# Kernel tuning notes

Measured on AMD Instinct MI355X. Metric: run time of the kernel, lower is better.

## Reference

```python
import jax, jax.numpy as jnp
import numpy as np

NUM_HEADS = 8


def setup_inputs() -> dict:
    key = jax.random.key(0)
    ks = jax.random.split(key, 14)
    B, S, E = 4, 2048, 512
    D_EMO = 64
    s = 1.0 / np.sqrt(E)
    inp = {
        "query": jax.random.normal(ks[0], (B, S, E), jnp.float32),
        "key": jax.random.normal(ks[1], (B, S, E), jnp.float32),
        "value": jax.random.normal(ks[2], (B, S, E), jnp.float32),
        "emotional_context": jax.random.normal(ks[3], (B, D_EMO), jnp.float32),
        "Wq": jax.random.normal(ks[4], (E, E), jnp.float32) * s,
        "bq": jnp.zeros((E,), jnp.float32),
        "Wk": jax.random.normal(ks[5], (E, E), jnp.float32) * s,
        "bk": jnp.zeros((E,), jnp.float32),
        "Wv": jax.random.normal(ks[6], (E, E), jnp.float32) * s,
        "bv": jnp.zeros((E,), jnp.float32),
        "Wo": jax.random.normal(ks[7], (E, E), jnp.float32) * s,
        "bo": jnp.zeros((E,), jnp.float32),
        "emo_bias": jax.random.normal(ks[8], (NUM_HEADS, 1, 1), jnp.float32),
    }
    return inp


def reference(query, key, value, emotional_context, Wq, bq, Wk, bk, Wv, bv, Wo, bo, emo_bias):
    B, S, E = query.shape
    H = NUM_HEADS
    D = E // H
    scale = 1.0 / np.sqrt(D).astype(np.float32)

    def proj(x, W, b):  # [B,S,E] -> [B,H,S,D]
        return (x @ W.T + b).reshape(B, S, H, D).transpose(0, 2, 1, 3)

    Q = proj(query, Wq, bq)
    K = proj(key, Wk, bk)
    V = proj(value, Wv, bv)

    # [B,H,S,S] score tensor (the memory-bound hot spot)
    scores = jnp.einsum("bhqd,bhkd->bhqk", Q, K) * scale
    scores = scores + emo_bias[None]  # additive per-head emotional bias
    # multiplicative emotional modulation: sigmoid of mean context, per batch
    mod = 0.5 + 0.5 * jax.nn.sigmoid(emotional_context.mean(axis=-1))  # [B]
    scores = scores * mod[:, None, None, None]

    attn = jax.nn.softmax(scores, axis=-1)
    # dropout(0.1) is identity in eval mode
    attended = jnp.einsum("bhqk,bhkd->bhqd", attn, V)
    attended = attended.transpose(0, 2, 1, 3).reshape(B, S, E)
    output = attended @ Wo.T + bo
    return output, attn.mean(axis=1)
```

## Files before the change

### kernel.cpp

```cpp
#include <hip/hip_runtime.h>

#define BATCH 4
#define SEQ   2048
#define EMB   512
#define HEADS 8
#define HD    64

typedef _Float16 half2_t __attribute__((ext_vector_type(2)));
typedef _Float16 half4_t __attribute__((ext_vector_type(4)));
typedef _Float16 half8_t __attribute__((ext_vector_type(8)));
typedef float    f32x4   __attribute__((ext_vector_type(4)));

#if __has_builtin(__builtin_amdgcn_exp2f)
#define EXP2F(x) __builtin_amdgcn_exp2f(x)
#else
#define EXP2F(x) exp2f(x)
#endif
#define LOG2E 1.44269504088896f

#define PKRTZ(a, b) __builtin_bit_cast(half2_t, __builtin_amdgcn_cvt_pkrtz((a), (b)))

__global__ void mod_kernel(const float* __restrict__ emo, float* __restrict__ modv){
    int lane = threadIdx.x;
    for (int b = 0; b < BATCH; ++b){
        float v = emo[b*64 + lane];
        #pragma unroll
        for (int off = 32; off >= 1; off >>= 1) v += __shfl_xor(v, off, 64);
        if (lane == 0){
            float mean = v * (1.0f/64.0f);
            float sig  = 1.0f/(1.0f + __expf(-mean));
            modv[b] = 0.5f + 0.5f*sig;
        }
    }
}

__device__ inline half8_t cvt8pk(float4 v0, float4 v1){
    half2_t p0 = PKRTZ(v0.x, v0.y), p1 = PKRTZ(v0.z, v0.w);
    half2_t p2 = PKRTZ(v1.x, v1.y), p3 = PKRTZ(v1.z, v1.w);
    half4_t a = __builtin_shufflevector(p0, p1, 0, 1, 2, 3);
    half4_t b = __builtin_shufflevector(p2, p3, 0, 1, 2, 3);
    return __builtin_shufflevector(a, b, 0, 1, 2, 3, 4, 5, 6, 7);
}
__device__ inline half8_t cvt8(const float* p){
    return cvt8pk(*(const float4*)p, *(const float4*)(p + 4));
}

__global__ __launch_bounds__(256) void qkv_kernel(
    const float* __restrict__ X0, const float* __restrict__ X1, const float* __restrict__ X2,
    const float* __restrict__ W0, const float* __restrict__ W1, const float* __restrict__ W2,
    const float* __restrict__ b0, const float* __restrict__ b1, const float* __restrict__ b2,
    _Float16* __restrict__ o0, _Float16* __restrict__ o1, _Float16* __restrict__ o2)
{
    const int z = blockIdx.z;
    const float* X    = (z==0) ? X0 : (z==1) ? X1 : X2;
    const float* W    = (z==0) ? W0 : (z==1) ? W1 : W2;
    const float* bias = (z==0) ? b0 : (z==1) ? b1 : b2;
    _Float16*  out    = (z==0) ? o0 : (z==1) ? o1 : o2;

    __shared__ _Float16 lA[128*64];
    __shared__ _Float16 lB[64*64];

    const int tid  = threadIdx.x;
    const int wid  = tid >> 6;
    const int lane = tid & 63;
    const int l16  = lane & 15;
    const int g    = lane >> 4;
    const int l7   = l16 & 7;
    const int mb = blockIdx.x;
    const int nb = blockIdx.y;
    const int wm = (wid >> 1)*64;
    const int wn = (wid & 1)*32;
    const int tR = tid >> 3;
    const int c8 = tid & 7;

    #pragma unroll
    for (int p = 0; p < 4; ++p){
        const int R = p*32 + tR;
        *(half8_t*)(lA + R*64 + ((c8 ^ (R & 7))*8)) = cvt8(X + (size_t)(mb*128 + R)*EMB + c8*8);
    }
    #pragma unroll
    for (int p = 0; p < 2; ++p){
        const int R = p*32 + tR;
        *(half8_t*)(lB + R*64 + ((c8 ^ (R & 7))*8)) = cvt8(W + (size_t)(nb*64 + R)*EMB + c8*8);
    }
    __syncthreads();

    f32x4 acc[4][2] = {};
    for (int ks = 0; ks < 8; ++ks){
        float4 xa0[4], xa1[4], wb0[2], wb1[2];
        if (ks < 7){
            #pragma unroll
            for (int p = 0; p < 4; ++p){
                const float* px = X + (size_t)(mb*128 + p*32 + tR)*EMB + (ks+1)*64 + c8*8;
                xa0[p] = *(const float4*)px;
                xa1[p] = *(const float4*)(px + 4);
            }
            #pragma unroll
            for (int p = 0; p < 2; ++p){
                const float* pw = W + (size_t)(nb*64 + p*32 + tR)*EMB + (ks+1)*64 + c8*8;
                wb0[p] = *(const float4*)pw;
                wb1[p] = *(const float4*)(pw + 4);
            }
        }
        __builtin_amdgcn_s_setprio(1);
        #pragma unroll
        for (int u = 0; u < 2; ++u){
            half8_t af[4], bf[2];
            #pragma unroll
            for (int i = 0; i < 4; ++i){
                const int rA = wm + i*16 + l16;
                af[i] = *(half8_t*)(lA + rA*64 + (((u*4 + g) ^ l7)*8));
            }
            #pragma unroll
            for (int j = 0; j < 2; ++j){
                const int rB = wn + j*16 + l16;
                bf[j] = *(half8_t*)(lB + rB*64 + (((u*4 + g) ^ l7)*8));
            }
            #pragma unroll
            for (int i = 0; i < 4; ++i)
                #pragma unroll
                for (int j = 0; j < 2; ++j)
                    acc[i][j] = __builtin_amdgcn_mfma_f32_16x16x32_f16(af[i], bf[j], acc[i][j], 0, 0, 0);
        }
        __builtin_amdgcn_s_setprio(0);
        __syncthreads();
        if (ks < 7){
            #pragma unroll
            for (int p = 0; p < 4; ++p){
                const int R = p*32 + tR;
                *(half8_t*)(lA + R*64 + ((c8 ^ (R & 7))*8)) = cvt8pk(xa0[p], xa1[p]);
            }
            #pragma unroll
            for (int p = 0; p < 2; ++p){
                const int R = p*32 + tR;
                *(half8_t*)(lB + R*64 + ((c8 ^ (R & 7))*8)) = cvt8pk(wb0[p], wb1[p]);
            }
            __syncthreads();
        }
    }
    #pragma unroll
    for (int j = 0; j < 2; ++j){
        const int nn  = nb*64 + wn + j*16 + l16;
        const float bn = bias[nn];
        const int h = nn >> 6, d = nn & 63;
        #pragma unroll
        for (int i = 0; i < 4; ++i){
            #pragma unroll
            for (int r = 0; r < 4; ++r){
                const int m  = mb*128 + wm + i*16 + 4*g + r;
                const int bb2 = m >> 11, s = m & 2047;
                const int bh  = bb2*8 + h;
                const float v = acc[i][j][r] + bn;
                size_t idx;
                if (z == 2)
                    idx = ((size_t)(bh*128 + (s>>4))*2 + (d>>5))*512
                        + (size_t)((((s>>2)&3)*16 + (d&15))*8 + ((d>>4)&1)*4 + (s&3));
                else
                    idx = ((size_t)(bh*128 + (s>>4))*2 + (d>>5))*512
                        + (size_t)((((d>>3)&3)*16 + (s&15))*8 + (d&7));
                out[idx] = (_Float16)v;
            }
        }
    }
}

__global__ __launch_bounds__(256) void pv_kernel(
    const _Float16* __restrict__ Qf, const _Float16* __restrict__ Kf,
    const _Float16* __restrict__ Vf, const float* __restrict__ emo_bias,
    const float* __restrict__ modv, _Float16* __restrict__ attended,
    float* __restrict__ Ldenom)
{
    __shared__ _Float16 lK[2][4096];
    __shared__ _Float16 lV[2][4096];

    const int tid  = threadIdx.x;
    const int lane = tid & 63;
    const int l16  = lane & 15;
    const int g    = lane >> 4;
    const int n    = blockIdx.x;
    const int work = (n & 7)*128 + (n >> 3);
    const int qt   = work & 31;
    const int bh   = work >> 5;
    const int b    = bh >> 3, h = bh & 7;
    const int q0   = qt*64 + (tid >> 6)*16;

    const float mod = modv[b];
    const float sm2 = 0.125f * mod * LOG2E;
    const float bm2 = emo_bias[h] * mod * LOG2E;

    const size_t fB = (size_t)bh * 128;

    half8_t qf[2];
    #pragma unroll
    for (int c = 0; c < 2; ++c)
        qf[c] = *(const half8_t*)(Qf + ((fB + (q0>>4))*2 + c)*512 + lane*8);

    {
        const _Float16* gk = Kf + fB*1024;
        const _Float16* gv = Vf + fB*1024;
        *(half8_t*)(&lK[0][tid*8])        = *(const half8_t*)(gk + tid*8);
        *(half8_t*)(&lK[0][2048 + tid*8]) = *(const half8_t*)(gk + 2048 + tid*8);
        *(half8_t*)(&lV[0][tid*8])        = *(const half8_t*)(gv + tid*8);
        *(half8_t*)(&lV[0][2048 + tid*8]) = *(const half8_t*)(gv + 2048 + tid*8);
    }
    __syncthreads();

    const half4_t ones4 = {(_Float16)1.0f, (_Float16)1.0f, (_Float16)1.0f, (_Float16)1.0f};
    f32x4 acc[4] = {};
    f32x4 acc5 = {};
    int cur = 0;
    for (int grp = 0; grp < SEQ/64; ++grp){
        half8_t rk0, rk1, rv0, rv1;
        if (grp < SEQ/64 - 1){
            const _Float16* gk = Kf + (fB + (size_t)(grp+1)*4)*1024;
            const _Float16* gv = Vf + (fB + (size_t)(grp+1)*4)*1024;
            rk0 = *(const half8_t*)(gk + tid*8);
            rk1 = *(const half8_t*)(gk + 2048 + tid*8);
            rv0 = *(const half8_t*)(gv + tid*8);
            rv1 = *(const half8_t*)(gv + 2048 + tid*8);
        }
        const _Float16* kb = &lK[cur][0];
        const _Float16* vb = &lV[cur][0];
        f32x4 s[4];
        __builtin_amdgcn_s_setprio(1);
        #pragma unroll
        for (int t = 0; t < 4; ++t){
            half8_t k0 = *(const half8_t*)(kb + (t*2+0)*512 + lane*8);
            half8_t k1 = *(const half8_t*)(kb + (t*2+1)*512 + lane*8);
            f32x4 zz = {};
            zz = __builtin_amdgcn_mfma_f32_16x16x32_f16(k0, qf[0], zz, 0, 0, 0);
            zz = __builtin_amdgcn_mfma_f32_16x16x32_f16(k1, qf[1], zz, 0, 0, 0);
            s[t] = zz;
        }
        __builtin_amdgcn_s_setprio(0);
        half4_t pf[4];
        #pragma unroll
        for (int t = 0; t < 4; ++t){
            float e0 = EXP2F(s[t][0]*sm2 + bm2);
            float e1 = EXP2F(s[t][1]*sm2 + bm2);
            float e2 = EXP2F(s[t][2]*sm2 + bm2);
            float e3 = EXP2F(s[t][3]*sm2 + bm2);
            half2_t plo = PKRTZ(e0, e1), phi = PKRTZ(e2, e3);
            pf[t] = __builtin_shufflevector(plo, phi, 0, 1, 2, 3);
        }
        __builtin_amdgcn_s_setprio(1);
        #pragma unroll
        for (int t = 0; t < 4; ++t){
            half8_t vp0 = *(const half8_t*)(vb + (t*2+0)*512 + lane*8);
            half8_t vp1 = *(const half8_t*)(vb + (t*2+1)*512 + lane*8);
            half4_t v0 = __builtin_shufflevector(vp0, vp0, 0, 1, 2, 3);
            half4_t v1 = __builtin_shufflevector(vp0, vp0, 4, 5, 6, 7);
            half4_t v2 = __builtin_shufflevector(vp1, vp1, 0, 1, 2, 3);
            half4_t v3 = __builtin_shufflevector(vp1, vp1, 4, 5, 6, 7);
            acc5   = __builtin_amdgcn_mfma_f32_16x16x16f16(pf[t], ones4, acc5, 0, 0, 0);
            acc[0] = __builtin_amdgcn_mfma_f32_16x16x16f16(pf[t], v0, acc[0], 0, 0, 0);
            acc[1] = __builtin_amdgcn_mfma_f32_16x16x16f16(pf[t], v1, acc[1], 0, 0, 0);
            acc[2] = __builtin_amdgcn_mfma_f32_16x16x16f16(pf[t], v2, acc[2], 0, 0, 0);
            acc[3] = __builtin_amdgcn_mfma_f32_16x16x16f16(pf[t], v3, acc[3], 0, 0, 0);
        }
        __builtin_amdgcn_s_setprio(0);
        if (grp < SEQ/64 - 1){
            *(half8_t*)(&lK[cur^1][tid*8])        = rk0;
            *(half8_t*)(&lK[cur^1][2048 + tid*8]) = rk1;
            *(half8_t*)(&lV[cur^1][tid*8])        = rv0;
            *(half8_t*)(&lV[cur^1][2048 + tid*8]) = rv1;
        }
        __syncthreads();
        cur ^= 1;
    }

    if (l16 == 0){
        #pragma unroll
        for (int r = 0; r < 4; ++r)
            Ldenom[(size_t)bh*SEQ + q0 + 4*g + r] = acc5[r];
    }
    float invr[4];
    #pragma unroll
    for (int r = 0; r < 4; ++r)
        invr[r] = 1.0f / acc5[r];
    #pragma unroll
    for (int c = 0; c < 4; ++c)
        #pragma unroll
        for (int r = 0; r < 4; ++r)
            attended[(size_t)(b*SEQ + q0 + 4*g + r)*EMB + h*64 + 16*c + l16]
                = (_Float16)(acc[c][r] * invr[r]);
}

__global__ __launch_bounds__(256) void mean_kernel(
    const _Float16* __restrict__ Qf, const _Float16* __restrict__ Kf,
    const float* __restrict__ emo_bias, const float* __restrict__ modv,
    const float* __restrict__ Ldenom, float* __restrict__ mean_out)
{
    const int tid  = threadIdx.x;
    const int w    = tid >> 6;
    const int lane = tid & 63;
    const int l16  = lane & 15;
    const int g    = lane >> 4;
    const int n    = blockIdx.x;
    const int work = (n & 7)*256 + (n >> 3);
    const int b    = work >> 9;
    const int ky   = (work >> 6) & 7;
    const int qt   = work & 63;
    const int q0   = qt * 32;
    const int k0w  = ky*256 + w*64;

    const float mod = modv[b];
    const float sm2 = 0.125f * mod * LOG2E;

    f32x4 msum[2][4] = {};
    for (int hp = 0; hp < HEADS/2; ++hp){
        const int h0 = 2*hp, h1 = 2*hp + 1;
        const size_t lo0 = (size_t)(b*HEADS + h0) * SEQ;
        const size_t lo1 = (size_t)(b*HEADS + h1) * SEQ;
        const size_t f0  = (size_t)(b*HEADS + h0) * 128;
        const size_t f1  = (size_t)(b*HEADS + h1) * 128;
        const float bm20 = emo_bias[h0] * mod * LOG2E;
        const float bm21 = emo_bias[h1] * mod * LOG2E;
        half8_t qA[2][2], qB[2][2];
        float elA[2][4], elB[2][4];
        #pragma unroll
        for (int T = 0; T < 2; ++T){
            const int qr = q0 + T*16;
            #pragma unroll
            for (int c = 0; c < 2; ++c){
                qA[T][c] = *(const half8_t*)(Qf + ((f0 + (qr>>4))*2 + c)*512 + lane*8);
                qB[T][c] = *(const half8_t*)(Qf + ((f1 + (qr>>4))*2 + c)*512 + lane*8);
            }
            #pragma unroll
            for (int r = 0; r < 4; ++r){
                elA[T][r] = bm20 - __log2f(Ldenom[lo0 + qr + 4*g + r]);
                elB[T][r] = bm21 - __log2f(Ldenom[lo1 + qr + 4*g + r]);
            }
        }
        #pragma unroll
        for (int j = 0; j < 4; ++j){
            const int kc = (k0w >> 4) + j;
            half8_t ka0 = *(const half8_t*)(Kf + ((f0 + kc)*2 + 0)*512 + lane*8);
            half8_t ka1 = *(const half8_t*)(Kf + ((f0 + kc)*2 + 1)*512 + lane*8);
            half8_t kb0 = *(const half8_t*)(Kf + ((f1 + kc)*2 + 0)*512 + lane*8);
            half8_t kb1 = *(const half8_t*)(Kf + ((f1 + kc)*2 + 1)*512 + lane*8);
            #pragma unroll
            for (int T = 0; T < 2; ++T){
                f32x4 sA = {}, sB = {};
                sA = __builtin_amdgcn_mfma_f32_16x16x32_f16(qA[T][0], ka0, sA, 0, 0, 0);
                sA = __builtin_amdgcn_mfma_f32_16x16x32_f16(qA[T][1], ka1, sA, 0, 0, 0);
                sB = __builtin_amdgcn_mfma_f32_16x16x32_f16(qB[T][0], kb0, sB, 0, 0, 0);
                sB = __builtin_amdgcn_mfma_f32_16x16x32_f16(qB[T][1], kb1, sB, 0, 0, 0);
                #pragma unroll
                for (int r = 0; r < 4; ++r)
                    msum[T][j][r] += EXP2F(sA[r]*sm2 + elA[T][r])
                                   + EXP2F(sB[r]*sm2 + elB[T][r]);
            }
        }
    }
    #pragma unroll
    for (int T = 0; T < 2; ++T)
        #pragma unroll
        for (int j = 0; j < 4; ++j)
            #pragma unroll
            for (int r = 0; r < 4; ++r)
                mean_out[(size_t)(b*SEQ + q0 + T*16 + 4*g + r)*SEQ + k0w + j*16 + l16]
                    = msum[T][j][r] * (1.0f/HEADS);
}

__global__ __launch_bounds__(256) void outproj_kernel(
    const _Float16* __restrict__ A, const float* __restrict__ W,
    const float* __restrict__ bias, float* __restrict__ out)
{
    __shared__ _Float16 lA[128*64];
    __shared__ _Float16 lB[64*64];

    const int tid  = threadIdx.x;
    const int wid  = tid >> 6;
    const int lane = tid & 63;
    const int l16  = lane & 15;
    const int g    = lane >> 4;
    const int l7   = l16 & 7;
    const int mb = blockIdx.x;
    const int nb = blockIdx.y;
    const int wm = (wid >> 1)*64;
    const int wn = (wid & 1)*32;
    const int tR = tid >> 3;
    const int c8 = tid & 7;

    #pragma unroll
    for (int p = 0; p < 4; ++p){
        const int R = p*32 + tR;
        *(half8_t*)(lA + R*64 + ((c8 ^ (R & 7))*8)) =
            *(const half8_t*)(A + (size_t)(mb*128 + R)*EMB + c8*8);
    }
    #pragma unroll
    for (int p = 0; p < 2; ++p){
        const int R = p*32 + tR;
        *(half8_t*)(lB + R*64 + ((c8 ^ (R & 7))*8)) = cvt8(W + (size_t)(nb*64 + R)*EMB + c8*8);
    }
    __syncthreads();

    f32x4 acc[4][2] = {};
    for (int ks = 0; ks < 8; ++ks){
        half8_t ra[4];
        float4 wb0[2], wb1[2];
        if (ks < 7){
            #pragma unroll
            for (int p = 0; p < 4; ++p)
                ra[p] = *(const half8_t*)(A + (size_t)(mb*128 + p*32 + tR)*EMB + (ks+1)*64 + c8*8);
            #pragma unroll
            for (int p = 0; p < 2; ++p){
                const float* pw = W + (size_t)(nb*64 + p*32 + tR)*EMB + (ks+1)*64 + c8*8;
                wb0[p] = *(const float4*)pw;
                wb1[p] = *(const float4*)(pw + 4);
            }
        }
        __builtin_amdgcn_s_setprio(1);
        #pragma unroll
        for (int u = 0; u < 2; ++u){
            half8_t af[4], bf[2];
            #pragma unroll
            for (int i = 0; i < 4; ++i){
                const int rA = wm + i*16 + l16;
                af[i] = *(half8_t*)(lA + rA*64 + (((u*4 + g) ^ l7)*8));
            }
            #pragma unroll
            for (int j = 0; j < 2; ++j){
                const int rB = wn + j*16 + l16;
                bf[j] = *(half8_t*)(lB + rB*64 + (((u*4 + g) ^ l7)*8));
            }
            #pragma unroll
            for (int i = 0; i < 4; ++i)
                #pragma unroll
                for (int j = 0; j < 2; ++j)
                    acc[i][j] = __builtin_amdgcn_mfma_f32_16x16x32_f16(af[i], bf[j], acc[i][j], 0, 0, 0);
        }
        __builtin_amdgcn_s_setprio(0);
        __syncthreads();
        if (ks < 7){
            #pragma unroll
            for (int p = 0; p < 4; ++p){
                const int R = p*32 + tR;
                *(half8_t*)(lA + R*64 + ((c8 ^ (R & 7))*8)) = ra[p];
            }
            #pragma unroll
            for (int p = 0; p < 2; ++p){
                const int R = p*32 + tR;
                *(half8_t*)(lB + R*64 + ((c8 ^ (R & 7))*8)) = cvt8pk(wb0[p], wb1[p]);
            }
            __syncthreads();
        }
    }
    #pragma unroll
    for (int j = 0; j < 2; ++j){
        const int nn = nb*64 + wn + j*16 + l16;
        const float bn = bias[nn];
        #pragma unroll
        for (int i = 0; i < 4; ++i)
            #pragma unroll
            for (int r = 0; r < 4; ++r){
                const int m = mb*128 + wm + i*16 + 4*g + r;
                out[(size_t)m*EMB + nn] = acc[i][j][r] + bn;
            }
    }
}

extern "C" void kernel_launch(void* const* d_in, const int* in_sizes, int n_in,
                              void* d_out, int out_size, void* d_ws, size_t ws_size,
                              hipStream_t stream)
{
    const float* query = (const float*)d_in[0];
    const float* key_  = (const float*)d_in[1];
    const float* value = (const float*)d_in[2];
    const float* emo   = (const float*)d_in[3];
    const float* Wq = (const float*)d_in[4];
    const float* bq = (const float*)d_in[5];
    const float* Wk = (const float*)d_in[6];
    const float* bk = (const float*)d_in[7];
    const float* Wv = (const float*)d_in[8];
    const float* bv = (const float*)d_in[9];
    const float* Wo = (const float*)d_in[10];
    const float* bo = (const float*)d_in[11];
    const float* emo_bias = (const float*)d_in[12];

    const size_t NTOK = (size_t)BATCH * SEQ * EMB;
    _Float16* ws       = (_Float16*)d_ws;
    _Float16* Qp       = ws;
    _Float16* Kp       = ws + NTOK;
    _Float16* Vt       = ws + 2*NTOK;
    _Float16* attended = ws + 3*NTOK;

    float* out0     = (float*)d_out;
    float* mean_out = out0 + NTOK;
    float* Ldenom   = out0;
    float* modv     = out0 + (size_t)BATCH*HEADS*SEQ;

    mod_kernel<<<1, 64, 0, stream>>>(emo, modv);
    qkv_kernel<<<dim3(64, 8, 3), 256, 0, stream>>>(query, key_, value, Wq, Wk, Wv,
                                                   bq, bk, bv, Qp, Kp, Vt);
    pv_kernel<<<BATCH*HEADS*(SEQ/64), 256, 0, stream>>>(Qp, Kp, Vt, emo_bias, modv, attended, Ldenom);
    mean_kernel<<<BATCH*(SEQ/32)*(SEQ/256), 256, 0, stream>>>(Qp, Kp, emo_bias, modv, Ldenom, mean_out);
    outproj_kernel<<<dim3(64, 8), 256, 0, stream>>>(attended, Wo, bo, out0);
}
```

Measured before the change: 162.5 us.

## Split PV attention over two key halves and combine partial sums

Splits the key sequence of the attention-value kernel into two halves, doubling the grid so each block handles half the keys with smaller LDS tiles. Each half writes unnormalized fp32 partial accumulators and denominators into scratch regions of the output buffer. A new combine kernel sums them, normalizes and writes the fp16 attended tensor and the denominators. This adds occupancy and parallelism (1024 to 2048 blocks) at the cost of an extra kernel launch and a round trip of fp32 partials through memory.

After: 169.7 us. 1.04x slower.

```diff
diff --git a/kernel.cpp b/kernel.cpp
--- a/kernel.cpp
+++ b/kernel.cpp
@@ -167,20 +167,21 @@
 __global__ __launch_bounds__(256) void pv_kernel(
     const _Float16* __restrict__ Qf, const _Float16* __restrict__ Kf,
     const _Float16* __restrict__ Vf, const float* __restrict__ emo_bias,
-    const float* __restrict__ modv, _Float16* __restrict__ attended,
-    float* __restrict__ Ldenom)
+    const float* __restrict__ modv, float* __restrict__ PA,
+    float* __restrict__ PL)
 {
-    __shared__ _Float16 lK[2][4096];
-    __shared__ _Float16 lV[2][4096];
+    __shared__ _Float16 lK[2][2048];
+    __shared__ _Float16 lV[2][2048];
 
     const int tid  = threadIdx.x;
     const int lane = tid & 63;
     const int l16  = lane & 15;
     const int g    = lane >> 4;
     const int n    = blockIdx.x;
-    const int work = (n & 7)*128 + (n >> 3);
-    const int qt   = work & 31;
-    const int bh   = work >> 5;
+    const int work = (n & 7)*256 + (n >> 3);
+    const int kh   = work & 1;
+    const int qt   = (work >> 1) & 31;
+    const int bh   = work >> 6;
     const int b    = bh >> 3, h = bh & 7;
     const int q0   = qt*64 + (tid >> 6)*16;
 
@@ -189,6 +190,7 @@
     const float bm2 = emo_bias[h] * mod * LOG2E;
 
     const size_t fB = (size_t)bh * 128;
+    const int tb0 = kh * 64;
 
     half8_t qf[2];
     #pragma unroll
@@ -196,12 +198,8 @@
         qf[c] = *(const half8_t*)(Qf + ((fB + (q0>>4))*2 + c)*512 + lane*8);
 
     {
-        const _Float16* gk = Kf + fB*1024;
-        const _Float16* gv = Vf + fB*1024;
-        *(half8_t*)(&lK[0][tid*8])        = *(const half8_t*)(gk + tid*8);
-        *(half8_t*)(&lK[0][2048 + tid*8]) = *(const half8_t*)(gk + 2048 + tid*8);
-        *(half8_t*)(&lV[0][tid*8])        = *(const half8_t*)(gv + tid*8);
-        *(half8_t*)(&lV[0][2048 + tid*8]) = *(const half8_t*)(gv + 2048 + tid*8);
+        *(half8_t*)(&lK[0][tid*8]) = *(const half8_t*)(Kf + (fB + tb0)*1024 + tid*8);
+        *(half8_t*)(&lV[0][tid*8]) = *(const half8_t*)(Vf + (fB + tb0)*1024 + tid*8);
     }
     __syncthreads();
 
@@ -209,22 +207,18 @@
     f32x4 acc[4] = {};
     f32x4 acc5 = {};
     int cur = 0;
-    for (int grp = 0; grp < SEQ/64; ++grp){
-        half8_t rk0, rk1, rv0, rv1;
-        if (grp < SEQ/64 - 1){
-            const _Float16* gk = Kf + (fB + (size_t)(grp+1)*4)*1024;
-            const _Float16* gv = Vf + (fB + (size_t)(grp+1)*4)*1024;
-            rk0 = *(const half8_t*)(gk + tid*8);
-            rk1 = *(const half8_t*)(gk + 2048 + tid*8);
-            rv0 = *(const half8_t*)(gv + tid*8);
-            rv1 = *(const half8_t*)(gv + 2048 + tid*8);
+    for (int grp = 0; grp < 32; ++grp){
+        half8_t rk, rv;
+        if (grp < 31){
+            rk = *(const half8_t*)(Kf + (fB + tb0 + (grp+1)*2)*1024 + tid*8);
+            rv = *(const half8_t*)(Vf + (fB + tb0 + (grp+1)*2)*1024 + tid*8);
         }
         const _Float16* kb = &lK[cur][0];
         const _Float16* vb = &lV[cur][0];
-        f32x4 s[4];
+        f32x4 s[2];
         __builtin_amdgcn_s_setprio(1);
         #pragma unroll
-        for (int t = 0; t < 4; ++t){
+        for (int t = 0; t < 2; ++t){
             half8_t k0 = *(const half8_t*)(kb + (t*2+0)*512 + lane*8);
             half8_t k1 = *(const half8_t*)(kb + (t*2+1)*512 + lane*8);
             f32x4 zz = {};
@@ -233,9 +227,9 @@
             s[t] = zz;
         }
         __builtin_amdgcn_s_setprio(0);
-        half4_t pf[4];
-        #pragma unroll
-        for (int t = 0; t < 4; ++t){
+        half4_t pf[2];
+        #pragma unroll
+        for (int t = 0; t < 2; ++t){
             float e0 = EXP2F(s[t][0]*sm2 + bm2);
             float e1 = EXP2F(s[t][1]*sm2 + bm2);
             float e2 = EXP2F(s[t][2]*sm2 + bm2);
@@ -245,7 +239,7 @@
         }
         __builtin_amdgcn_s_setprio(1);
         #pragma unroll
-        for (int t = 0; t < 4; ++t){
+        for (int t = 0; t < 2; ++t){
             half8_t vp0 = *(const half8_t*)(vb + (t*2+0)*512 + lane*8);
             half8_t vp1 = *(const half8_t*)(vb + (t*2+1)*512 + lane*8);
             half4_t v0 = __builtin_shufflevector(vp0, vp0, 0, 1, 2, 3);
@@ -259,31 +253,49 @@
             acc[3] = __builtin_amdgcn_mfma_f32_16x16x16f16(pf[t], v3, acc[3], 0, 0, 0);
         }
         __builtin_amdgcn_s_setprio(0);
-        if (grp < SEQ/64 - 1){
-            *(half8_t*)(&lK[cur^1][tid*8])        = rk0;
-            *(half8_t*)(&lK[cur^1][2048 + tid*8]) = rk1;
-            *(half8_t*)(&lV[cur^1][tid*8])        = rv0;
-            *(half8_t*)(&lV[cur^1][2048 + tid*8]) = rv1;
+        if (grp < 31){
+            *(half8_t*)(&lK[cur^1][tid*8]) = rk;
+            *(half8_t*)(&lV[cur^1][tid*8]) = rv;
         }
         __syncthreads();
         cur ^= 1;
     }
 
-    if (l16 == 0){
-        #pragma unroll
-        for (int r = 0; r < 4; ++r)
-            Ldenom[(size_t)bh*SEQ + q0 + 4*g + r] = acc5[r];
-    }
-    float invr[4];
-    #pragma unroll
-    for (int r = 0; r < 4; ++r)
-        invr[r] = 1.0f / acc5[r];
-    #pragma unroll
-    for (int c = 0; c < 4; ++c)
-        #pragma unroll
-        for (int r = 0; r < 4; ++r)
-            attended[(size_t)(b*SEQ + q0 + 4*g + r)*EMB + h*64 + 16*c + l16]
-                = (_Float16)(acc[c][r] * invr[r]);
+    const size_t base = (size_t)kh * (32u*SEQ) ;
+    #pragma unroll
+    for (int r = 0; r < 4; ++r){
+        const size_t row = base + (size_t)bh*SEQ + q0 + 4*g + r;
+        #pragma unroll
+        for (int c = 0; c < 4; ++c)
+            PA[row*64 + 16*c + l16] = acc[c][r];
+        if (l16 == 0) PL[row] = acc5[r];
+    }
+}
+
+__global__ __launch_bounds__(256) void combine_kernel(
+    const float* __restrict__ PA, const float* __restrict__ PL,
+    _Float16* __restrict__ attended, float* __restrict__ Ldenom)
+{
+    const size_t NROW = (size_t)BATCH*HEADS*SEQ;
+    const size_t gid  = (size_t)blockIdx.x*256 + threadIdx.x;
+    const size_t base = gid*8;
+    const size_t row  = base >> 6;
+    const int    d0   = (int)(base & 63);
+    if (row >= NROW) return;
+    const int bh = (int)(row >> 11), q = (int)(row & 2047);
+    const int b = bh >> 3, h = bh & 7;
+
+    const float L = PL[row] + PL[NROW + row];
+    const float inv = 1.0f / L;
+    float4 a0 = *(const float4*)(PA + row*64 + d0);
+    float4 a1 = *(const float4*)(PA + row*64 + d0 + 4);
+    float4 b0 = *(const float4*)(PA + NROW*64 + row*64 + d0);
+    float4 b1 = *(const float4*)(PA + NROW*64 + row*64 + d0 + 4);
+    float4 s0, s1;
+    s0.x=(a0.x+b0.x)*inv; s0.y=(a0.y+b0.y)*inv; s0.z=(a0.z+b0.z)*inv; s0.w=(a0.w+b0.w)*inv;
+    s1.x=(a1.x+b1.x)*inv; s1.y=(a1.y+b1.y)*inv; s1.z=(a1.z+b1.z)*inv; s1.w=(a1.w+b1.w)*inv;
+    *(half8_t*)(attended + ((size_t)(b*SEQ + q))*EMB + h*64 + d0) = cvt8pk(s0, s1);
+    if (d0 == 0) Ldenom[row] = L;
 }
 
 __global__ __launch_bounds__(256) void mean_kernel(
@@ -488,13 +500,16 @@
 
     float* out0     = (float*)d_out;
     float* mean_out = out0 + NTOK;
-    float* Ldenom   = out0;
-    float* modv     = out0 + (size_t)BATCH*HEADS*SEQ;
+    float* Ldenom = out0;
+    float* modv   = out0 + (size_t)BATCH*HEADS*SEQ;
+    float* PL     = out0 + 262144;
+    float* PA     = mean_out;
 
     mod_kernel<<<1, 64, 0, stream>>>(emo, modv);
     qkv_kernel<<<dim3(64, 8, 3), 256, 0, stream>>>(query, key_, value, Wq, Wk, Wv,
                                                    bq, bk, bv, Qp, Kp, Vt);
-    pv_kernel<<<BATCH*HEADS*(SEQ/64), 256, 0, stream>>>(Qp, Kp, Vt, emo_bias, modv, attended, Ldenom);
+    pv_kernel<<<BATCH*HEADS*(SEQ/64)*2, 256, 0, stream>>>(Qp, Kp, Vt, emo_bias, modv, PA, PL);
+    combine_kernel<<<(BATCH*HEADS*SEQ*HD/8 + 255)/256, 256, 0, stream>>>(PA, PL, attended, Ldenom);
     mean_kernel<<<BATCH*(SEQ/32)*(SEQ/256), 256, 0, stream>>>(Qp, Kp, emo_bias, modv, Ldenom, mean_out);
     outproj_kernel<<<dim3(64, 8), 256, 0, stream>>>(attended, Wo, bo, out0);
 }
```
